# Performance work log

Hardware: AMD Instinct MI355X
Metric: run time of the kernel (lower is better)

Reference implementation:

```python
import jax, jax.numpy as jnp
import numpy as np

B, NW, H, K = 64, 256, 768, 4
K1, Bp, AVDL = 0.1, 1.2, 50.0
ALPHA = 1.0 / H  # 1 / interaction_rep_size
BETA = 0.1


def setup_inputs() -> dict:
    key = jax.random.key(0)
    k1, k2, k3, k4, k5, k6 = jax.random.split(key, 6)
    return {
        "q_rep": jax.random.normal(k1, (B, NW, H), dtype=jnp.float32),
        "d_rep": jax.random.normal(k2, (B, NW, H), dtype=jnp.float32),
        "qtw": jax.random.uniform(k3, (B, NW), dtype=jnp.float32),
        "q_input_ids": jax.random.randint(k4, (B, NW, K), 0, 32, dtype=jnp.int32),
        "d_input_ids": jax.random.randint(k5, (B, NW, K), 0, 32, dtype=jnp.int32),
        "d_tfs": jax.random.randint(k6, (B, NW), 0, 10, dtype=jnp.int32),
    }


def _null_mask(input_ids):
    # [B, NW, 1] float mask: 0 where the whole window is zero ids
    all_zero = jnp.all(input_ids == 0, axis=2)
    return (~all_zero).astype(jnp.float32)[:, :, None]


def reference(q_rep, d_rep, qtw, q_input_ids, d_input_ids, d_tfs):
    q = q_rep * _null_mask(q_input_ids)
    d = d_rep * _null_mask(d_input_ids)

    # term-overlap scores: [B, NW, NW]
    d_expanded_tf = jnp.einsum("bqh,bdh->bqd", q, d)

    # exact match between q windows and d windows: [B, NW, NW]
    em_f = jnp.all(q_input_ids[:, :, None, :] == d_input_ids[:, None, :, :],
                   axis=3).astype(jnp.float32)

    # blended expanded term frequency, weighted by doc term frequencies
    d_tf = d_expanded_tf * (ALPHA * BETA) + em_f * (1.0 - BETA)
    tf_mult = d_tfs.astype(jnp.float32)[:, None, :]          # [B, 1, NW]
    expanded_term_df = jnp.sum(d_tf * tf_mult, axis=2)       # [B, NW]

    # BM25-like scoring
    dl = jnp.sum(d_tfs.astype(jnp.float32), axis=1, keepdims=True)  # [B, 1]
    denom = expanded_term_df * (1.0 + K1)
    nom = expanded_term_df + K1 * (1.0 - Bp + Bp * dl / AVDL)
    dtw = denom / (nom + 1e-8)
    s = jnp.sum(qtw * dtw, axis=1)                           # [B]
    return s, d_expanded_tf
```

## Files before the change

### kernel.cpp

```cpp
#include <hip/hip_runtime.h>
#include <hip/hip_bf16.h>

#define B_   64
#define NW_  256
#define H_   768

#define ALPHA_BETA     (0.1f / 768.0f)
#define ONE_MINUS_BETA 0.9f
#define K1_            0.1f
#define BP_            1.2f
#define AVDL_          50.0f

typedef __bf16 bf16x8 __attribute__((ext_vector_type(8)));
typedef float  f32x4  __attribute__((ext_vector_type(4)));

__global__ __launch_bounds__(64) void gemm_kernel(
    const float* __restrict__ q_rep, const float* __restrict__ d_rep,
    const int* __restrict__ q_ids, const int* __restrict__ d_ids,
    float* __restrict__ S)
{
    __shared__ __align__(16) __bf16 As[2][64][40];
    __shared__ __align__(16) __bf16 Bs[2][64][40];

    const int lane = threadIdx.x;
    const int b  = blockIdx.z;
    const int m0 = blockIdx.y * 64;
    const int n0 = blockIdx.x * 64;

    const int rq  = lane >> 2;
    const int seg = lane & 3;

    float mA[4], mB[4];
#pragma unroll
    for (int it = 0; it < 4; ++it) {
        const int row = it * 16 + rq;
        int4 qa = *(const int4*)(q_ids + ((size_t)b * NW_ + m0 + row) * 4);
        mA[it] = (qa.x == 0 && qa.y == 0 && qa.z == 0 && qa.w == 0) ? 0.f : 1.f;
        int4 da = *(const int4*)(d_ids + ((size_t)b * NW_ + n0 + row) * 4);
        mB[it] = (da.x == 0 && da.y == 0 && da.z == 0 && da.w == 0) ? 0.f : 1.f;
    }

    const float* Abase = q_rep + ((size_t)b * NW_ + m0) * H_;
    const float* Bbase = d_rep + ((size_t)b * NW_ + n0) * H_;

    f32x4 acc[4][4];
#pragma unroll
    for (int i = 0; i < 4; ++i)
#pragma unroll
        for (int j = 0; j < 4; ++j)
            acc[i][j] = (f32x4){0.f, 0.f, 0.f, 0.f};

    float4 ra[8], rb[8];

    auto load_tiles = [&](int k0) {
#pragma unroll
        for (int it = 0; it < 4; ++it) {
            const float* pa = Abase + (size_t)(it * 16 + rq) * H_ + k0 + seg * 8;
            ra[it * 2]     = *(const float4*)pa;
            ra[it * 2 + 1] = *(const float4*)(pa + 4);
            const float* pb = Bbase + (size_t)(it * 16 + rq) * H_ + k0 + seg * 8;
            rb[it * 2]     = *(const float4*)pb;
            rb[it * 2 + 1] = *(const float4*)(pb + 4);
        }
    };

    auto write_tiles = [&](int buf) {
#pragma unroll
        for (int it = 0; it < 4; ++it) {
            const int row = it * 16 + rq;
            float4 x = ra[it * 2], y = ra[it * 2 + 1];
            float m = mA[it];
            bf16x8 va;
            va[0] = (__bf16)(x.x * m); va[1] = (__bf16)(x.y * m);
            va[2] = (__bf16)(x.z * m); va[3] = (__bf16)(x.w * m);
            va[4] = (__bf16)(y.x * m); va[5] = (__bf16)(y.y * m);
            va[6] = (__bf16)(y.z * m); va[7] = (__bf16)(y.w * m);
            *(bf16x8*)&As[buf][row][seg * 8] = va;

            float4 u = rb[it * 2], v = rb[it * 2 + 1];
            float n = mB[it];
            bf16x8 vb;
            vb[0] = (__bf16)(u.x * n); vb[1] = (__bf16)(u.y * n);
            vb[2] = (__bf16)(u.z * n); vb[3] = (__bf16)(u.w * n);
            vb[4] = (__bf16)(v.x * n); vb[5] = (__bf16)(v.y * n);
            vb[6] = (__bf16)(v.z * n); vb[7] = (__bf16)(v.w * n);
            *(bf16x8*)&Bs[buf][row][seg * 8] = vb;
        }
    };

    const int fr = lane & 15;
    const int fk = (lane >> 4) * 8;

    auto compute = [&](int buf) {
        bf16x8 af[4], bfr[4];
#pragma unroll
        for (int t = 0; t < 4; ++t) {
            af[t]  = *(bf16x8*)&As[buf][t * 16 + fr][fk];
            bfr[t] = *(bf16x8*)&Bs[buf][t * 16 + fr][fk];
        }
#pragma unroll
        for (int i = 0; i < 4; ++i)
#pragma unroll
            for (int j = 0; j < 4; ++j)
                acc[i][j] = __builtin_amdgcn_mfma_f32_16x16x32_bf16(
                    af[i], bfr[j], acc[i][j], 0, 0, 0);
    };

    load_tiles(0);
    write_tiles(0);
    int buf = 0;

    for (int kc = 1; kc < 24; ++kc) {
        __syncthreads();
        load_tiles(kc * 32);
        compute(buf);
        write_tiles(buf ^ 1);
        buf ^= 1;
    }
    __syncthreads();
    compute(buf);

    const int cn = lane & 15;
    const int rb4 = (lane >> 4) * 4;
#pragma unroll
    for (int i = 0; i < 4; ++i)
#pragma unroll
        for (int j = 0; j < 4; ++j)
#pragma unroll
            for (int r = 0; r < 4; ++r) {
                const int m = m0 + i * 16 + rb4 + r;
                const int n = n0 + j * 16 + cn;
                S[((size_t)b * NW_ + m) * NW_ + n] = acc[i][j][r];
            }
}

__global__ __launch_bounds__(64) void score_kernel(
    const float* __restrict__ S, const int* __restrict__ q_ids,
    const int* __restrict__ d_ids, const int* __restrict__ d_tfs,
    const float* __restrict__ qtw, float* __restrict__ ws_dtw)
{
    const int lane = threadIdx.x;
    const int q = blockIdx.x;
    const int b = blockIdx.y;

    int4 qk = *(const int4*)(q_ids + ((size_t)b * NW_ + q) * 4);

    const float* Srow = S + ((size_t)b * NW_ + q) * NW_;
    float4 sv  = *(const float4*)(Srow + lane * 4);
    int4  tf4  = *(const int4*)(d_tfs + (size_t)b * NW_ + lane * 4);
    const int4* dk = (const int4*)(d_ids + ((size_t)b * NW_ + lane * 4) * 4);

    float svv[4] = {sv.x, sv.y, sv.z, sv.w};
    float tfv[4] = {(float)tf4.x, (float)tf4.y, (float)tf4.z, (float)tf4.w};

    float s1 = 0.f, s2 = 0.f, s3 = 0.f;
#pragma unroll
    for (int j = 0; j < 4; ++j) {
        int4 dj = dk[j];
        bool em = (dj.x == qk.x) && (dj.y == qk.y) &&
                  (dj.z == qk.z) && (dj.w == qk.w);
        s1 += svv[j] * tfv[j];
        s2 += em ? tfv[j] : 0.f;
        s3 += tfv[j];
    }
#pragma unroll
    for (int off = 32; off; off >>= 1) {
        s1 += __shfl_xor(s1, off);
        s2 += __shfl_xor(s2, off);
        s3 += __shfl_xor(s3, off);
    }
    if (lane == 0) {
        float etdf = ALPHA_BETA * s1 + ONE_MINUS_BETA * s2;
        float dl = s3;
        float c = K1_ * (1.f - BP_ + BP_ * dl / AVDL_);
        float dtw = (etdf * (1.f + K1_)) / (etdf + c + 1e-8f);
        ws_dtw[(size_t)b * NW_ + q] = qtw[(size_t)b * NW_ + q] * dtw;
    }
}

__global__ __launch_bounds__(64) void final_kernel(
    const float* __restrict__ ws_dtw, float* __restrict__ out)
{
    const int b = blockIdx.x;
    const int lane = threadIdx.x;
    float4 v = *(const float4*)(ws_dtw + (size_t)b * NW_ + lane * 4);
    float s = v.x + v.y + v.z + v.w;
#pragma unroll
    for (int off = 32; off; off >>= 1) s += __shfl_xor(s, off);
    if (lane == 0) out[b] = s;
}

extern "C" void kernel_launch(void* const* d_in, const int* in_sizes, int n_in,
                              void* d_out, int out_size, void* d_ws, size_t ws_size,
                              hipStream_t stream)
{
    const float* q_rep = (const float*)d_in[0];
    const float* d_rep = (const float*)d_in[1];
    const float* qtw   = (const float*)d_in[2];
    const int*   q_ids = (const int*)d_in[3];
    const int*   d_ids = (const int*)d_in[4];
    const int*   d_tfs = (const int*)d_in[5];

    float* out = (float*)d_out;
    float* S   = out + B_;
    float* ws_dtw = (float*)d_ws;

    dim3 ggrid(NW_ / 64, NW_ / 64, B_);
    gemm_kernel<<<ggrid, 64, 0, stream>>>(q_rep, d_rep, q_ids, d_ids, S);

    dim3 sgrid(NW_, B_);
    score_kernel<<<sgrid, 64, 0, stream>>>(S, q_ids, d_ids, d_tfs, qtw, ws_dtw);

    final_kernel<<<B_, 64, 0, stream>>>(ws_dtw, out);
}
```

Before: 178.3 us.

## Fuse score epilogue into GEMM with split-K across four waves

```diff
diff --git a/kernel.cpp b/kernel.cpp
--- a/kernel.cpp
+++ b/kernel.cpp
@@ -6,7 +6,7 @@
 #define H_   768
 
 #define ALPHA_BETA     (0.1f / 768.0f)
-#define ONE_MINUS_BETA 0.9f
+#define OMB_           0.9f
 #define K1_            0.1f
 #define BP_            1.2f
 #define AVDL_          50.0f
@@ -14,18 +14,23 @@
 typedef __bf16 bf16x8 __attribute__((ext_vector_type(8)));
 typedef float  f32x4  __attribute__((ext_vector_type(4)));
 
-__global__ __launch_bounds__(64) void gemm_kernel(
+__global__ __launch_bounds__(256, 4) void gemm_score_kernel(
     const float* __restrict__ q_rep, const float* __restrict__ d_rep,
     const int* __restrict__ q_ids, const int* __restrict__ d_ids,
-    float* __restrict__ S)
+    const int* __restrict__ d_tfs,
+    float* __restrict__ S, float* __restrict__ ws_etdf)
 {
-    __shared__ __align__(16) __bf16 As[2][64][40];
-    __shared__ __align__(16) __bf16 Bs[2][64][40];
-
-    const int lane = threadIdx.x;
+    __shared__ __align__(16) unsigned char lds[40960];
+
+    const int tid  = threadIdx.x;
+    const int wave = tid >> 6;
+    const int lane = tid & 63;
     const int b  = blockIdx.z;
     const int m0 = blockIdx.y * 64;
     const int n0 = blockIdx.x * 64;
+
+    __bf16* As = (__bf16*)(lds + wave * 10240);
+    __bf16* Bs = As + 64 * 40;
 
     const int rq  = lane >> 2;
     const int seg = lane & 3;
@@ -40,8 +45,8 @@
         mB[it] = (da.x == 0 && da.y == 0 && da.z == 0 && da.w == 0) ? 0.f : 1.f;
     }
 
-    const float* Abase = q_rep + ((size_t)b * NW_ + m0) * H_;
-    const float* Bbase = d_rep + ((size_t)b * NW_ + n0) * H_;
+    const float* Abase = q_rep + ((size_t)b * NW_ + m0) * H_ + wave * 192;
+    const float* Bbase = d_rep + ((size_t)b * NW_ + n0) * H_ + wave * 192;
 
     f32x4 acc[4][4];
 #pragma unroll
@@ -50,21 +55,20 @@
         for (int j = 0; j < 4; ++j)
             acc[i][j] = (f32x4){0.f, 0.f, 0.f, 0.f};
 
-    float4 ra[8], rb[8];
-
-    auto load_tiles = [&](int k0) {
+    const int fr = lane & 15;
+    const int fk = (lane >> 4) * 8;
+
+    for (int kc = 0; kc < 6; ++kc) {
+        float4 ra[8], rb[8];
 #pragma unroll
         for (int it = 0; it < 4; ++it) {
-            const float* pa = Abase + (size_t)(it * 16 + rq) * H_ + k0 + seg * 8;
+            const float* pa = Abase + (size_t)(it * 16 + rq) * H_ + kc * 32 + seg * 8;
             ra[it * 2]     = *(const float4*)pa;
             ra[it * 2 + 1] = *(const float4*)(pa + 4);
-            const float* pb = Bbase + (size_t)(it * 16 + rq) * H_ + k0 + seg * 8;
+            const float* pb = Bbase + (size_t)(it * 16 + rq) * H_ + kc * 32 + seg * 8;
             rb[it * 2]     = *(const float4*)pb;
             rb[it * 2 + 1] = *(const float4*)(pb + 4);
         }
-    };
-
-    auto write_tiles = [&](int buf) {
 #pragma unroll
         for (int it = 0; it < 4; ++it) {
             const int row = it * 16 + rq;
@@ -75,7 +79,7 @@
             va[2] = (__bf16)(x.z * m); va[3] = (__bf16)(x.w * m);
             va[4] = (__bf16)(y.x * m); va[5] = (__bf16)(y.y * m);
             va[6] = (__bf16)(y.z * m); va[7] = (__bf16)(y.w * m);
-            *(bf16x8*)&As[buf][row][seg * 8] = va;
+            *(bf16x8*)&As[row * 40 + seg * 8] = va;
 
             float4 u = rb[it * 2], v = rb[it * 2 + 1];
             float n = mB[it];
@@ -84,19 +88,13 @@
             vb[2] = (__bf16)(u.z * n); vb[3] = (__bf16)(u.w * n);
             vb[4] = (__bf16)(v.x * n); vb[5] = (__bf16)(v.y * n);
             vb[6] = (__bf16)(v.z * n); vb[7] = (__bf16)(v.w * n);
-            *(bf16x8*)&Bs[buf][row][seg * 8] = vb;
-        }
-    };
-
-    const int fr = lane & 15;
-    const int fk = (lane >> 4) * 8;
-
-    auto compute = [&](int buf) {
+            *(bf16x8*)&Bs[row * 40 + seg * 8] = vb;
+        }
         bf16x8 af[4], bfr[4];
 #pragma unroll
         for (int t = 0; t < 4; ++t) {
-            af[t]  = *(bf16x8*)&As[buf][t * 16 + fr][fk];
-            bfr[t] = *(bf16x8*)&Bs[buf][t * 16 + fr][fk];
+            af[t]  = *(bf16x8*)&As[(t * 16 + fr) * 40 + fk];
+            bfr[t] = *(bf16x8*)&Bs[(t * 16 + fr) * 40 + fk];
         }
 #pragma unroll
         for (int i = 0; i < 4; ++i)
@@ -104,87 +102,87 @@
             for (int j = 0; j < 4; ++j)
                 acc[i][j] = __builtin_amdgcn_mfma_f32_16x16x32_bf16(
                     af[i], bfr[j], acc[i][j], 0, 0, 0);
-    };
-
-    load_tiles(0);
-    write_tiles(0);
-    int buf = 0;
-
-    for (int kc = 1; kc < 24; ++kc) {
+    }
+
+    __syncthreads();
+
+    float* T     = (float*)lds;
+    int4*  qk_s  = (int4*)(lds + 17408);
+    int4*  dk_s  = (int4*)(lds + 18432);
+    float* tf_s  = (float*)(lds + 19456);
+
+    if (tid < 64)
+        qk_s[tid] = *(const int4*)(q_ids + ((size_t)b * NW_ + m0 + tid) * 4);
+    else if (tid < 128)
+        dk_s[tid - 64] = *(const int4*)(d_ids + ((size_t)b * NW_ + n0 + tid - 64) * 4);
+    else if (tid < 192)
+        tf_s[tid - 128] = (float)d_tfs[(size_t)b * NW_ + n0 + tid - 128];
+
+    const int cn  = lane & 15;
+    const int rb4 = (lane >> 4) * 4;
+    for (int w = 0; w < 4; ++w) {
+        if (wave == w) {
+#pragma unroll
+            for (int i = 0; i < 4; ++i)
+#pragma unroll
+                for (int j = 0; j < 4; ++j)
+#pragma unroll
+                    for (int r = 0; r < 4; ++r) {
+                        const int row = i * 16 + rb4 + r;
+                        const int col = j * 16 + cn;
+                        if (w == 0) T[row * 68 + col]  = acc[i][j][r];
+                        else        T[row * 68 + col] += acc[i][j][r];
+                    }
+        }
         __syncthreads();
-        load_tiles(kc * 32);
-        compute(buf);
-        write_tiles(buf ^ 1);
-        buf ^= 1;
-    }
-    __syncthreads();
-    compute(buf);
-
-    const int cn = lane & 15;
-    const int rb4 = (lane >> 4) * 4;
+    }
+
+    const int r  = tid >> 2;
+    const int qq = tid & 3;
+    const float* Tr = &T[r * 68 + qq * 16];
+    float* Srow = S + ((size_t)b * NW_ + m0 + r) * NW_ + n0 + qq * 16;
 #pragma unroll
     for (int i = 0; i < 4; ++i)
-#pragma unroll
-        for (int j = 0; j < 4; ++j)
-#pragma unroll
-            for (int r = 0; r < 4; ++r) {
-                const int m = m0 + i * 16 + rb4 + r;
-                const int n = n0 + j * 16 + cn;
-                S[((size_t)b * NW_ + m) * NW_ + n] = acc[i][j][r];
-            }
+        ((float4*)Srow)[i] = ((const float4*)Tr)[i];
+
+    int4 qk = qk_s[r];
+    float ps = 0.f;
+#pragma unroll
+    for (int i = 0; i < 16; ++i) {
+        const int c = qq * 16 + i;
+        int4 dk = dk_s[c];
+        float em = (dk.x == qk.x && dk.y == qk.y &&
+                    dk.z == qk.z && dk.w == qk.w) ? OMB_ : 0.f;
+        ps += (ALPHA_BETA * Tr[i] + em) * tf_s[c];
+    }
+    ps += __shfl_xor(ps, 1);
+    ps += __shfl_xor(ps, 2);
+    if (qq == 0)
+        atomicAdd(&ws_etdf[(size_t)b * NW_ + m0 + r], ps);
 }
 
-__global__ __launch_bounds__(64) void score_kernel(
-    const float* __restrict__ S, const int* __restrict__ q_ids,
-    const int* __restrict__ d_ids, const int* __restrict__ d_tfs,
-    const float* __restrict__ qtw, float* __restrict__ ws_dtw)
-{
-    const int lane = threadIdx.x;
-    const int q = blockIdx.x;
-    const int b = blockIdx.y;
-
-    int4 qk = *(const int4*)(q_ids + ((size_t)b * NW_ + q) * 4);
-
-    const float* Srow = S + ((size_t)b * NW_ + q) * NW_;
-    float4 sv  = *(const float4*)(Srow + lane * 4);
-    int4  tf4  = *(const int4*)(d_tfs + (size_t)b * NW_ + lane * 4);
-    const int4* dk = (const int4*)(d_ids + ((size_t)b * NW_ + lane * 4) * 4);
-
-    float svv[4] = {sv.x, sv.y, sv.z, sv.w};
-    float tfv[4] = {(float)tf4.x, (float)tf4.y, (float)tf4.z, (float)tf4.w};
-
-    float s1 = 0.f, s2 = 0.f, s3 = 0.f;
-#pragma unroll
-    for (int j = 0; j < 4; ++j) {
-        int4 dj = dk[j];
-        bool em = (dj.x == qk.x) && (dj.y == qk.y) &&
-                  (dj.z == qk.z) && (dj.w == qk.w);
-        s1 += svv[j] * tfv[j];
-        s2 += em ? tfv[j] : 0.f;
-        s3 += tfv[j];
-    }
-#pragma unroll
-    for (int off = 32; off; off >>= 1) {
-        s1 += __shfl_xor(s1, off);
-        s2 += __shfl_xor(s2, off);
-        s3 += __shfl_xor(s3, off);
-    }
-    if (lane == 0) {
-        float etdf = ALPHA_BETA * s1 + ONE_MINUS_BETA * s2;
-        float dl = s3;
-        float c = K1_ * (1.f - BP_ + BP_ * dl / AVDL_);
-        float dtw = (etdf * (1.f + K1_)) / (etdf + c + 1e-8f);
-        ws_dtw[(size_t)b * NW_ + q] = qtw[(size_t)b * NW_ + q] * dtw;
-    }
-}
-
 __global__ __launch_bounds__(64) void final_kernel(
-    const float* __restrict__ ws_dtw, float* __restrict__ out)
+    const float* __restrict__ ws_etdf, const int* __restrict__ d_tfs,
+    const float* __restrict__ qtw, float* __restrict__ out)
 {
     const int b = blockIdx.x;
     const int lane = threadIdx.x;
-    float4 v = *(const float4*)(ws_dtw + (size_t)b * NW_ + lane * 4);
-    float s = v.x + v.y + v.z + v.w;
+
+    float4 ev = *(const float4*)(ws_etdf + (size_t)b * NW_ + lane * 4);
+    int4  tf4 = *(const int4*)(d_tfs   + (size_t)b * NW_ + lane * 4);
+    float4 qv = *(const float4*)(qtw    + (size_t)b * NW_ + lane * 4);
+
+    float dl = (float)(tf4.x + tf4.y + tf4.z + tf4.w);
+#pragma unroll
+    for (int off = 32; off; off >>= 1) dl += __shfl_xor(dl, off);
+
+    const float c = K1_ * (1.f - BP_ + BP_ * dl / AVDL_);
+    float ew[4] = {ev.x, ev.y, ev.z, ev.w};
+    float qw[4] = {qv.x, qv.y, qv.z, qv.w};
+    float s = 0.f;
+#pragma unroll
+    for (int j = 0; j < 4; ++j)
+        s += qw[j] * (ew[j] * (1.f + K1_)) / (ew[j] + c + 1e-8f);
 #pragma unroll
     for (int off = 32; off; off >>= 1) s += __shfl_xor(s, off);
     if (lane == 0) out[b] = s;
@@ -203,13 +201,13 @@
 
     float* out = (float*)d_out;
     float* S   = out + B_;
-    float* ws_dtw = (float*)d_ws;
+    float* ws_etdf = (float*)d_ws;
+
+    hipMemsetAsync(ws_etdf, 0, (size_t)B_ * NW_ * sizeof(float), stream);
 
     dim3 ggrid(NW_ / 64, NW_ / 64, B_);
-    gemm_kernel<<<ggrid, 64, 0, stream>>>(q_rep, d_rep, q_ids, d_ids, S);
-
-    dim3 sgrid(NW_, B_);
-    score_kernel<<<sgrid, 64, 0, stream>>>(S, q_ids, d_ids, d_tfs, qtw, ws_dtw);
-
-    final_kernel<<<B_, 64, 0, stream>>>(ws_dtw, out);
+    gemm_score_kernel<<<ggrid, 256, 0, stream>>>(q_rep, d_rep, q_ids, d_ids,
+                                                 d_tfs, S, ws_etdf);
+
+    final_kernel<<<B_, 64, 0, stream>>>(ws_etdf, d_tfs, qtw, out);
 }
```

Result: faster. 171.3 us (-3.9%).
